# Optimization experiments

Hardware: AMD Instinct MI355X
Metric: run time of the kernel (lower is better)

The kernel has to match this reference:

```python
import jax, jax.numpy as jnp
import numpy as np

# column-index constants for the node feature matrix and edge attributes
VM, VA, PG, QG, PD, QD = 0, 1, 2, 3, 4, 5
G_COL, B_COL = 0, 1

N_NODES = 100000
N_EDGES = 3200000
N_FEAT = 6


def setup_inputs() -> dict:
    key = jax.random.key(0)
    k1, k2, k3, k4, k5, k6 = jax.random.split(key, 6)
    pred = jax.random.normal(k1, (N_NODES, N_FEAT), dtype=jnp.float32)
    target = jax.random.normal(k2, (N_NODES, N_FEAT), dtype=jnp.float32)
    src = jax.random.randint(k3, (N_EDGES,), 0, N_NODES, dtype=jnp.int32)
    dst = jax.random.randint(k4, (N_EDGES,), 0, N_NODES, dtype=jnp.int32)
    edge_index = jnp.stack([src, dst], axis=0)
    edge_attr = jax.random.normal(k5, (N_EDGES, 2), dtype=jnp.float32)
    mask = jax.random.bernoulli(k6, 0.5, (N_NODES, N_FEAT))
    return {"pred": pred, "target": target, "edge_index": edge_index,
            "edge_attr": edge_attr, "mask": mask}


def reference(pred, target, edge_index, edge_attr, mask):
    # temp_pred[~mask] = target[~mask]
    tp = jnp.where(mask, pred, target)

    V_m = tp[:, VM]
    V_a = tp[:, VA]
    V = V_m * jnp.exp(1j * V_a)           # complex64 [N]
    V_conj = jnp.conj(V)

    # conj(Y_bus) entries on edges: G - jB
    Y_conj = edge_attr[:, G_COL] - 1j * edge_attr[:, B_COL]  # complex64 [E]

    row, col = edge_index[0], edge_index[1]
    # (Y_bus_conj @ V_conj)[i] = sum over edges (i,j) of conj(Y_ij) * conj(V_j)
    msg = Y_conj * V_conj[col]                               # gather-multiply [E]
    matvec = jax.ops.segment_sum(msg, row, num_segments=tp.shape[0])  # scatter-add [N]

    S_injection = V * matvec                                  # diag(V) @ (...)

    net_P = tp[:, PG] - tp[:, PD]
    net_Q = tp[:, QG] - tp[:, QD]
    diff = (net_P + 1j * net_Q) - S_injection

    loss = jnp.mean(jnp.abs(diff))
    real_loss = jnp.mean(jnp.abs(jnp.real(diff)))
    imag_loss = jnp.mean(jnp.abs(jnp.imag(diff)))
    return (loss, real_loss, imag_loss)
```

## Files before the change

### kernel.cpp

```cpp
#include <hip/hip_runtime.h>
#include <hip/hip_fp16.h>
#include <math.h>

constexpr int N_NODES = 100000;
constexpr int N_EDGES = 3200000;
constexpr int NF      = 6;

constexpr int BSHIFT  = 10;
constexpr int BNODES  = 1 << BSHIFT;
constexpr int NB      = (N_NODES + BNODES - 1) >> BSHIFT;
constexpr int CAP     = 33792;
constexpr int NSLICE  = 8;
constexpr int TILE    = 2048;
constexpr int EPT     = TILE / 256;
constexpr int NBLK_PART = (N_EDGES + TILE - 1) / TILE;
constexpr int VPREP_BLOCKS = (N_NODES + 255) / 256;

constexpr size_t MV_BYTES = (size_t)NB * BNODES * 8;
constexpr size_t OFF_V    = 0;
constexpr size_t OFF_A    = OFF_V + (size_t)N_NODES * 8;
constexpr size_t OFF_L    = OFF_A + (size_t)NB * CAP * 8;
constexpr size_t OFF_MV   = OFF_L + (size_t)NB * CAP * 2;
constexpr size_t OFF_CNT  = OFF_MV + MV_BYTES;
constexpr size_t WS_NEED  = OFF_CNT + 1024;

union F2U { float2 f; unsigned long long u; };

__global__ __launch_bounds__(256) void node_prep(
        const float* __restrict__ pred,
        const float* __restrict__ target,
        const unsigned char* __restrict__ mask,
        float2* __restrict__ v,
        float* __restrict__ mv) {
    int i = blockIdx.x * blockDim.x + threadIdx.x;
    for (int k = i; k < NB * BNODES * 2; k += VPREP_BLOCKS * 256)
        mv[k] = 0.f;
    if (i >= N_NODES) return;
    const int b = i * NF;
    float vm = mask[b + 0] ? pred[b + 0] : target[b + 0];
    float va = mask[b + 1] ? pred[b + 1] : target[b + 1];
    float s, c;
    sincosf(va, &s, &c);
    v[i] = make_float2(vm * c, vm * s);
}

__global__ __launch_bounds__(256) void partition_edges(
        const int* __restrict__ row, const int* __restrict__ col,
        const float2* __restrict__ attr,
        const float2* __restrict__ v,
        unsigned int* __restrict__ gcur,
        float2* __restrict__ Ag,
        unsigned short* __restrict__ Lg) {
    __shared__ unsigned int h[4][NB];
    __shared__ unsigned int cur[4][NB];
    __shared__ int wb[4][NB];
    __shared__ int dbase[NB];
    __shared__ unsigned int tot_s[NB];
    __shared__ float2 rec_s[TILE];
    __shared__ unsigned short li_s[TILE];
    __shared__ unsigned char bkt_s[TILE];
    __shared__ int total_s;

    const int tid = threadIdx.x;
    const int w = tid >> 6;
    const int e0 = blockIdx.x * TILE;
    const int e_base = e0 + tid * EPT;
    const bool ok = e_base < N_EDGES;

    for (int i = tid; i < 4 * NB; i += 256) {
        (&h[0][0])[i] = 0u;
        (&cur[0][0])[i] = 0u;
    }
    __syncthreads();

    int r[EPT];
    if (ok) {
        int4 ra = *(const int4*)(row + e_base);
        int4 rb = *(const int4*)(row + e_base + 4);
        r[0]=ra.x; r[1]=ra.y; r[2]=ra.z; r[3]=ra.w;
        r[4]=rb.x; r[5]=rb.y; r[6]=rb.z; r[7]=rb.w;
        #pragma unroll
        for (int k = 0; k < EPT; ++k)
            atomicAdd(&h[w][r[k] >> BSHIFT], 1u);
    }
    __syncthreads();

    if (tid < NB)
        tot_s[tid] = h[0][tid] + h[1][tid] + h[2][tid] + h[3][tid];
    __syncthreads();

    if (tid < NB) {
        int lbase = 0;
        for (int j = 0; j < tid; ++j) lbase += (int)tot_s[j];
        unsigned t0 = h[0][tid], t1 = h[1][tid], t2 = h[2][tid];
        unsigned tot = tot_s[tid];
        unsigned g = tot ? atomicAdd(&gcur[tid], tot) : 0u;
        dbase[tid] = (int)g - lbase;
        wb[0][tid] = lbase;
        wb[1][tid] = lbase + (int)t0;
        wb[2][tid] = lbase + (int)(t0 + t1);
        wb[3][tid] = lbase + (int)(t0 + t1 + t2);
        if (tid == NB - 1) total_s = lbase + (int)tot;
    }
    __syncthreads();

    if (ok) {
        int4 ca = *(const int4*)(col + e_base);
        int4 cb = *(const int4*)(col + e_base + 4);
        int c[EPT] = {ca.x, ca.y, ca.z, ca.w, cb.x, cb.y, cb.z, cb.w};
        float2 vv[EPT];
        #pragma unroll
        for (int k = 0; k < EPT; ++k) vv[k] = v[c[k]];
        float4 a0 = *(const float4*)(attr + e_base);
        float4 a1 = *(const float4*)(attr + e_base + 2);
        float4 a2 = *(const float4*)(attr + e_base + 4);
        float4 a3 = *(const float4*)(attr + e_base + 6);
        float gx[EPT] = {a0.x, a0.z, a1.x, a1.z, a2.x, a2.z, a3.x, a3.z};
        float gy[EPT] = {a0.y, a0.w, a1.y, a1.w, a2.y, a2.w, a3.y, a3.w};
        #pragma unroll
        for (int k = 0; k < EPT; ++k) {
            int rr = r[k];
            int b = rr >> BSHIFT;
            int slot = wb[w][b] + (int)atomicAdd(&cur[w][b], 1u);
            float mre = fmaf(gx[k], vv[k].x, -gy[k] * vv[k].y);
            float mim = -fmaf(gx[k], vv[k].y, gy[k] * vv[k].x);
            rec_s[slot] = make_float2(mre, mim);
            li_s[slot]  = (unsigned short)(rr & (BNODES - 1));
            bkt_s[slot] = (unsigned char)b;
        }
    }
    __syncthreads();

    const int total = total_s;
    for (int j = tid; j < total; j += 256) {
        int b = (int)bkt_s[j];
        int g = dbase[b] + j;
        if (g < CAP) {
            size_t o = (size_t)b * CAP + g;
            Ag[o] = rec_s[j];
            Lg[o] = li_s[j];
        }
    }
}

__global__ __launch_bounds__(256) void accum_finalize(
        const unsigned int* __restrict__ gcur,
        const float2* __restrict__ Ag,
        const unsigned short* __restrict__ Lg,
        float* __restrict__ mv,
        unsigned int* __restrict__ sdone,
        float* __restrict__ sums,
        unsigned int* __restrict__ done_all,
        const float* __restrict__ pred,
        const float* __restrict__ target,
        const unsigned char* __restrict__ mask,
        const float2* __restrict__ v,
        float* __restrict__ out) {
    __shared__ float acc_re[BNODES];
    __shared__ float acc_im[BNODES];
    __shared__ unsigned int old_s;
    const int tid = threadIdx.x;
    const int b = blockIdx.x / NSLICE;
    const int s = blockIdx.x % NSLICE;
    int cnt = (int)min(gcur[b], (unsigned)CAP);
    for (int i = tid; i < BNODES; i += 256) { acc_re[i] = 0.f; acc_im[i] = 0.f; }
    __syncthreads();
    int per = (((cnt + NSLICE - 1) / NSLICE) + 3) & ~3;
    int st = s * per;
    int en = min(st + per, cnt);
    const float2* ap = Ag + (size_t)b * CAP;
    const unsigned short* lp = Lg + (size_t)b * CAP;
    int j = st + 4 * tid;
    for (; j + 3 < en; j += 1024) {
        float4 m01 = *(const float4*)(ap + j);
        float4 m23 = *(const float4*)(ap + j + 2);
        ushort4 l4 = *(const ushort4*)(lp + j);
        atomicAdd(&acc_re[l4.x], m01.x);
        atomicAdd(&acc_im[l4.x], m01.y);
        atomicAdd(&acc_re[l4.y], m01.z);
        atomicAdd(&acc_im[l4.y], m01.w);
        atomicAdd(&acc_re[l4.z], m23.x);
        atomicAdd(&acc_im[l4.z], m23.y);
        atomicAdd(&acc_re[l4.w], m23.z);
        atomicAdd(&acc_im[l4.w], m23.w);
    }
    for (; j < en; ++j) {
        float2 m = ap[j];
        int li = (int)lp[j];
        atomicAdd(&acc_re[li], m.x);
        atomicAdd(&acc_im[li], m.y);
    }
    __syncthreads();
    {
        float* mvb = mv + (((size_t)b << BSHIFT) << 1);
        for (int i = tid; i < BNODES; i += 256) {
            float r = acc_re[i];
            float q = acc_im[i];
            if (r != 0.f || q != 0.f) {
                atomicAdd(&mvb[2 * i],     r);
                atomicAdd(&mvb[2 * i + 1], q);
            }
        }
    }
    asm volatile("s_waitcnt vmcnt(0)" ::: "memory");
    __syncthreads();
    if (tid == 0)
        old_s = __hip_atomic_fetch_add(&sdone[b], 1u, __ATOMIC_RELAXED,
                                       __HIP_MEMORY_SCOPE_AGENT);
    __syncthreads();
    if (old_s != (unsigned)(NSLICE - 1)) return;

    const unsigned long long* pb =
        reinterpret_cast<const unsigned long long*>(mv) + ((size_t)b << BSHIFT);
    float a = 0.f, ar = 0.f, ai = 0.f;
    for (int li = tid; li < BNODES; li += 256) {
        int i = (b << BSHIFT) + li;
        if (i >= N_NODES) break;
        F2U cvt;
        cvt.u = __hip_atomic_load(&pb[li], __ATOMIC_RELAXED,
                                  __HIP_MEMORY_SCOPE_AGENT);
        float mr = cvt.f.x, mi = cvt.f.y;
        const int bb = i * NF;
        float pg = mask[bb + 2] ? pred[bb + 2] : target[bb + 2];
        float qg = mask[bb + 3] ? pred[bb + 3] : target[bb + 3];
        float pd = mask[bb + 4] ? pred[bb + 4] : target[bb + 4];
        float qd = mask[bb + 5] ? pred[bb + 5] : target[bb + 5];
        float netP = pg - pd;
        float netQ = qg - qd;
        float2 vv = v[i];
        float s_re = vv.x * mr - vv.y * mi;
        float s_im = vv.x * mi + vv.y * mr;
        float dre = netP - s_re;
        float dim = netQ - s_im;
        ar += fabsf(dre);
        ai += fabsf(dim);
        a  += sqrtf(dre * dre + dim * dim);
    }
    #pragma unroll
    for (int off = 32; off > 0; off >>= 1) {
        a  += __shfl_down(a,  off, 64);
        ar += __shfl_down(ar, off, 64);
        ai += __shfl_down(ai, off, 64);
    }
    __shared__ float red[3][4];
    int wave = tid >> 6;
    int lane = tid & 63;
    if (lane == 0) { red[0][wave] = a; red[1][wave] = ar; red[2][wave] = ai; }
    __syncthreads();
    if (tid == 0) {
        float r0 = atomicAdd(&sums[0], red[0][0] + red[0][1] + red[0][2] + red[0][3]);
        float r1 = atomicAdd(&sums[1], red[1][0] + red[1][1] + red[1][2] + red[1][3]);
        float r2 = atomicAdd(&sums[2], red[2][0] + red[2][1] + red[2][2] + red[2][3]);
        float chk = r0 + r1 + r2;
        if (chk == chk) {
            unsigned fin = atomicAdd(done_all, 1u);
            if (fin == (unsigned)(NB - 1)) {
                const float inv = 1.0f / (float)N_NODES;
                float t0 = atomicAdd(&sums[0], 0.f);
                float t1 = atomicAdd(&sums[1], 0.f);
                float t2 = atomicAdd(&sums[2], 0.f);
                __hip_atomic_store(&out[0], t0 * inv, __ATOMIC_RELAXED, __HIP_MEMORY_SCOPE_AGENT);
                __hip_atomic_store(&out[1], t1 * inv, __ATOMIC_RELAXED, __HIP_MEMORY_SCOPE_AGENT);
                __hip_atomic_store(&out[2], t2 * inv, __ATOMIC_RELAXED, __HIP_MEMORY_SCOPE_AGENT);
            }
        }
    }
}

__global__ void node_prep_fb(const float* __restrict__ pred,
                             const float* __restrict__ target,
                             const unsigned char* __restrict__ mask,
                             float2* __restrict__ v) {
    int i = blockIdx.x * blockDim.x + threadIdx.x;
    if (i >= N_NODES) return;
    const int b = i * NF;
    float vm = mask[b + 0] ? pred[b + 0] : target[b + 0];
    float va = mask[b + 1] ? pred[b + 1] : target[b + 1];
    float s, c;
    sincosf(va, &s, &c);
    v[i] = make_float2(vm * c, vm * s);
}

__global__ void edge_scatter_fb(const int* __restrict__ row,
                                const int* __restrict__ col,
                                const float2* __restrict__ attr,
                                const float2* __restrict__ v,
                                float2* __restrict__ mv) {
    int e = blockIdx.x * blockDim.x + threadIdx.x;
    if (e >= N_EDGES) return;
    int r = row[e];
    int c = col[e];
    float2 gb = attr[e];
    float2 vv = v[c];
    float mre = fmaf(gb.x, vv.x, -gb.y * vv.y);
    float mim = -fmaf(gb.x, vv.y, gb.y * vv.x);
    atomicAdd(&mv[r].x, mre);
    atomicAdd(&mv[r].y, mim);
}

__global__ void finalize_fb(const float* __restrict__ pred,
                            const float* __restrict__ target,
                            const unsigned char* __restrict__ mask,
                            const float2* __restrict__ v,
                            const float2* __restrict__ mv,
                            float* __restrict__ sums) {
    int i = blockIdx.x * blockDim.x + threadIdx.x;
    float a = 0.f, ar = 0.f, ai = 0.f;
    if (i < N_NODES) {
        const int b = i * NF;
        float pg = mask[b + 2] ? pred[b + 2] : target[b + 2];
        float qg = mask[b + 3] ? pred[b + 3] : target[b + 3];
        float pd = mask[b + 4] ? pred[b + 4] : target[b + 4];
        float qd = mask[b + 5] ? pred[b + 5] : target[b + 5];
        float netP = pg - pd;
        float netQ = qg - qd;
        float2 vv = v[i];
        float2 m = mv[i];
        float s_re = vv.x * m.x - vv.y * m.y;
        float s_im = vv.x * m.y + vv.y * m.x;
        float dre = netP - s_re;
        float dim = netQ - s_im;
        ar = fabsf(dre);
        ai = fabsf(dim);
        a  = sqrtf(dre * dre + dim * dim);
    }
    #pragma unroll
    for (int off = 32; off > 0; off >>= 1) {
        a  += __shfl_down(a,  off, 64);
        ar += __shfl_down(ar, off, 64);
        ai += __shfl_down(ai, off, 64);
    }
    __shared__ float red[3][4];
    int wave = threadIdx.x >> 6;
    int lane = threadIdx.x & 63;
    if (lane == 0) { red[0][wave] = a; red[1][wave] = ar; red[2][wave] = ai; }
    __syncthreads();
    if (threadIdx.x == 0) {
        atomicAdd(&sums[0], red[0][0] + red[0][1] + red[0][2] + red[0][3]);
        atomicAdd(&sums[1], red[1][0] + red[1][1] + red[1][2] + red[1][3]);
        atomicAdd(&sums[2], red[2][0] + red[2][1] + red[2][2] + red[2][3]);
    }
}

__global__ void write_out_fb(const float* __restrict__ sums, float* __restrict__ out) {
    if (threadIdx.x == 0 && blockIdx.x == 0) {
        const float inv = 1.0f / (float)N_NODES;
        out[0] = sums[0] * inv;
        out[1] = sums[1] * inv;
        out[2] = sums[2] * inv;
    }
}

extern "C" void kernel_launch(void* const* d_in, const int* in_sizes, int n_in,
                              void* d_out, int out_size, void* d_ws, size_t ws_size,
                              hipStream_t stream) {
    const float*         pred   = (const float*)d_in[0];
    const float*         target = (const float*)d_in[1];
    const int*           eidx   = (const int*)d_in[2];
    const float2*        attr   = (const float2*)d_in[3];
    const unsigned char* mask   = (const unsigned char*)d_in[4];
    float* out = (float*)d_out;

    const int* row = eidx;
    const int* col = eidx + N_EDGES;

    char* ws = (char*)d_ws;
    const int B = 256;

    if (ws_size >= WS_NEED) {
        float2*             v        = (float2*)(ws + OFF_V);
        float2*             Ag       = (float2*)(ws + OFF_A);
        unsigned short*     Lg       = (unsigned short*)(ws + OFF_L);
        float*              mv       = (float*)(ws + OFF_MV);
        unsigned int*       gcur     = (unsigned int*)(ws + OFF_CNT);
        unsigned int*       sdone    = (unsigned int*)(ws + OFF_CNT + 512);
        float*              sums     = (float*)(ws + OFF_CNT + 912);
        unsigned int*       done_all = (unsigned int*)(ws + OFF_CNT + 928);

        hipMemsetAsync(ws + OFF_CNT, 0, 1024, stream);
        node_prep<<<VPREP_BLOCKS, B, 0, stream>>>(pred, target, mask, v, mv);
        partition_edges<<<NBLK_PART, B, 0, stream>>>(row, col, attr, v,
                                                     gcur, Ag, Lg);
        accum_finalize<<<NB * NSLICE, B, 0, stream>>>(gcur, Ag, Lg, mv,
                                                      sdone, sums, done_all,
                                                      pred, target, mask, v, out);
    } else {
        float2* v    = (float2*)ws;
        float2* mv   = (float2*)(ws + (size_t)N_NODES * 8);
        float*  sums = (float*)(ws + 2ull * N_NODES * 8);
        hipMemsetAsync(mv, 0, (size_t)N_NODES * 8 + 16, stream);
        node_prep_fb<<<(N_NODES + B - 1) / B, B, 0, stream>>>(pred, target, mask, v);
        edge_scatter_fb<<<(N_EDGES + B - 1) / B, B, 0, stream>>>(row, col, attr, v, mv);
        finalize_fb<<<(N_NODES + B - 1) / B, B, 0, stream>>>(pred, target, mask, v, mv, sums);
        write_out_fb<<<1, 64, 0, stream>>>(sums, out);
    }
}
```

Before: 195.7 us.

## Replace bucketed edge partitioning with direct global float atomics scatter

Drops the two-pass scheme that bucketed edges by row block into a workspace and then reduced each bucket with LDS atomics. Each edge now computes its message and adds it straight into the global matvec using unsafeAtomicAdd (hardware float atomics). A separate per-node finalize kernel then does the reduction. The memset is removed and node loads are vectorised. This avoids writing and re-reading the staged buffer, but it sends about 6.4M random global atomics through L2.

```diff
diff --git a/kernel.cpp b/kernel.cpp
--- a/kernel.cpp
+++ b/kernel.cpp
@@ -1,240 +1,110 @@
 #include <hip/hip_runtime.h>
-#include <hip/hip_fp16.h>
 #include <math.h>
 
 constexpr int N_NODES = 100000;
 constexpr int N_EDGES = 3200000;
 constexpr int NF      = 6;
 
-constexpr int BSHIFT  = 10;
-constexpr int BNODES  = 1 << BSHIFT;
-constexpr int NB      = (N_NODES + BNODES - 1) >> BSHIFT;
-constexpr int CAP     = 33792;
-constexpr int NSLICE  = 8;
-constexpr int TILE    = 2048;
-constexpr int EPT     = TILE / 256;
-constexpr int NBLK_PART = (N_EDGES + TILE - 1) / TILE;
-constexpr int VPREP_BLOCKS = (N_NODES + 255) / 256;
-
-constexpr size_t MV_BYTES = (size_t)NB * BNODES * 8;
-constexpr size_t OFF_V    = 0;
-constexpr size_t OFF_A    = OFF_V + (size_t)N_NODES * 8;
-constexpr size_t OFF_L    = OFF_A + (size_t)NB * CAP * 8;
-constexpr size_t OFF_MV   = OFF_L + (size_t)NB * CAP * 2;
-constexpr size_t OFF_CNT  = OFF_MV + MV_BYTES;
-constexpr size_t WS_NEED  = OFF_CNT + 1024;
-
-union F2U { float2 f; unsigned long long u; };
+constexpr int EPT       = 4;
+constexpr int NP_BLOCKS = (N_NODES + 255) / 256;
+constexpr int ES_BLOCKS = (N_EDGES / EPT + 255) / 256;
+
+constexpr size_t OFF_V   = 0;
+constexpr size_t OFF_MV  = OFF_V  + (size_t)N_NODES * 8;
+constexpr size_t OFF_CNT = OFF_MV + (size_t)N_NODES * 8;
+constexpr size_t WS_NEED = OFF_CNT + 64;
+
+__device__ __forceinline__ void fadd_atomic(float* p, float v) {
+#if defined(__HIP_PLATFORM_AMD__)
+    unsafeAtomicAdd(p, v);
+#else
+    atomicAdd(p, v);
+#endif
+}
 
 __global__ __launch_bounds__(256) void node_prep(
         const float* __restrict__ pred,
         const float* __restrict__ target,
         const unsigned char* __restrict__ mask,
         float2* __restrict__ v,
-        float* __restrict__ mv) {
-    int i = blockIdx.x * blockDim.x + threadIdx.x;
-    for (int k = i; k < NB * BNODES * 2; k += VPREP_BLOCKS * 256)
-        mv[k] = 0.f;
+        float2* __restrict__ mv,
+        unsigned int* __restrict__ cnt) {
+    int i = blockIdx.x * 256 + threadIdx.x;
+    if (i < 8) cnt[i] = 0u;
     if (i >= N_NODES) return;
+    mv[i] = make_float2(0.f, 0.f);
     const int b = i * NF;
-    float vm = mask[b + 0] ? pred[b + 0] : target[b + 0];
-    float va = mask[b + 1] ? pred[b + 1] : target[b + 1];
+    uchar2 m01 = *(const uchar2*)(mask + b);
+    float2 p01 = *(const float2*)(pred + b);
+    float2 t01 = *(const float2*)(target + b);
+    float vm = m01.x ? p01.x : t01.x;
+    float va = m01.y ? p01.y : t01.y;
     float s, c;
     sincosf(va, &s, &c);
     v[i] = make_float2(vm * c, vm * s);
 }
 
-__global__ __launch_bounds__(256) void partition_edges(
-        const int* __restrict__ row, const int* __restrict__ col,
+__global__ __launch_bounds__(256) void edge_scatter(
+        const int* __restrict__ row,
+        const int* __restrict__ col,
         const float2* __restrict__ attr,
         const float2* __restrict__ v,
-        unsigned int* __restrict__ gcur,
-        float2* __restrict__ Ag,
-        unsigned short* __restrict__ Lg) {
-    __shared__ unsigned int h[4][NB];
-    __shared__ unsigned int cur[4][NB];
-    __shared__ int wb[4][NB];
-    __shared__ int dbase[NB];
-    __shared__ unsigned int tot_s[NB];
-    __shared__ float2 rec_s[TILE];
-    __shared__ unsigned short li_s[TILE];
-    __shared__ unsigned char bkt_s[TILE];
-    __shared__ int total_s;
-
-    const int tid = threadIdx.x;
-    const int w = tid >> 6;
-    const int e0 = blockIdx.x * TILE;
-    const int e_base = e0 + tid * EPT;
-    const bool ok = e_base < N_EDGES;
-
-    for (int i = tid; i < 4 * NB; i += 256) {
-        (&h[0][0])[i] = 0u;
-        (&cur[0][0])[i] = 0u;
-    }
-    __syncthreads();
-
-    int r[EPT];
-    if (ok) {
-        int4 ra = *(const int4*)(row + e_base);
-        int4 rb = *(const int4*)(row + e_base + 4);
-        r[0]=ra.x; r[1]=ra.y; r[2]=ra.z; r[3]=ra.w;
-        r[4]=rb.x; r[5]=rb.y; r[6]=rb.z; r[7]=rb.w;
-        #pragma unroll
-        for (int k = 0; k < EPT; ++k)
-            atomicAdd(&h[w][r[k] >> BSHIFT], 1u);
-    }
-    __syncthreads();
-
-    if (tid < NB)
-        tot_s[tid] = h[0][tid] + h[1][tid] + h[2][tid] + h[3][tid];
-    __syncthreads();
-
-    if (tid < NB) {
-        int lbase = 0;
-        for (int j = 0; j < tid; ++j) lbase += (int)tot_s[j];
-        unsigned t0 = h[0][tid], t1 = h[1][tid], t2 = h[2][tid];
-        unsigned tot = tot_s[tid];
-        unsigned g = tot ? atomicAdd(&gcur[tid], tot) : 0u;
-        dbase[tid] = (int)g - lbase;
-        wb[0][tid] = lbase;
-        wb[1][tid] = lbase + (int)t0;
-        wb[2][tid] = lbase + (int)(t0 + t1);
-        wb[3][tid] = lbase + (int)(t0 + t1 + t2);
-        if (tid == NB - 1) total_s = lbase + (int)tot;
-    }
-    __syncthreads();
-
-    if (ok) {
-        int4 ca = *(const int4*)(col + e_base);
-        int4 cb = *(const int4*)(col + e_base + 4);
-        int c[EPT] = {ca.x, ca.y, ca.z, ca.w, cb.x, cb.y, cb.z, cb.w};
-        float2 vv[EPT];
-        #pragma unroll
-        for (int k = 0; k < EPT; ++k) vv[k] = v[c[k]];
-        float4 a0 = *(const float4*)(attr + e_base);
-        float4 a1 = *(const float4*)(attr + e_base + 2);
-        float4 a2 = *(const float4*)(attr + e_base + 4);
-        float4 a3 = *(const float4*)(attr + e_base + 6);
-        float gx[EPT] = {a0.x, a0.z, a1.x, a1.z, a2.x, a2.z, a3.x, a3.z};
-        float gy[EPT] = {a0.y, a0.w, a1.y, a1.w, a2.y, a2.w, a3.y, a3.w};
-        #pragma unroll
-        for (int k = 0; k < EPT; ++k) {
-            int rr = r[k];
-            int b = rr >> BSHIFT;
-            int slot = wb[w][b] + (int)atomicAdd(&cur[w][b], 1u);
-            float mre = fmaf(gx[k], vv[k].x, -gy[k] * vv[k].y);
-            float mim = -fmaf(gx[k], vv[k].y, gy[k] * vv[k].x);
-            rec_s[slot] = make_float2(mre, mim);
-            li_s[slot]  = (unsigned short)(rr & (BNODES - 1));
-            bkt_s[slot] = (unsigned char)b;
-        }
-    }
-    __syncthreads();
-
-    const int total = total_s;
-    for (int j = tid; j < total; j += 256) {
-        int b = (int)bkt_s[j];
-        int g = dbase[b] + j;
-        if (g < CAP) {
-            size_t o = (size_t)b * CAP + g;
-            Ag[o] = rec_s[j];
-            Lg[o] = li_s[j];
-        }
-    }
-}
-
-__global__ __launch_bounds__(256) void accum_finalize(
-        const unsigned int* __restrict__ gcur,
-        const float2* __restrict__ Ag,
-        const unsigned short* __restrict__ Lg,
-        float* __restrict__ mv,
-        unsigned int* __restrict__ sdone,
-        float* __restrict__ sums,
-        unsigned int* __restrict__ done_all,
+        float2* __restrict__ mv) {
+    int t = blockIdx.x * 256 + threadIdx.x;
+    int e = t * EPT;
+    if (e >= N_EDGES) return;
+    int4   r4  = *(const int4*)(row + e);
+    int4   c4  = *(const int4*)(col + e);
+    float4 a01 = *(const float4*)(attr + e);
+    float4 a23 = *(const float4*)(attr + e + 2);
+    float2 v0 = v[c4.x];
+    float2 v1 = v[c4.y];
+    float2 v2 = v[c4.z];
+    float2 v3 = v[c4.w];
+    float* m = (float*)mv;
+    fadd_atomic(&m[2 * r4.x],      fmaf(a01.x, v0.x, -a01.y * v0.y));
+    fadd_atomic(&m[2 * r4.x + 1], -fmaf(a01.x, v0.y,  a01.y * v0.x));
+    fadd_atomic(&m[2 * r4.y],      fmaf(a01.z, v1.x, -a01.w * v1.y));
+    fadd_atomic(&m[2 * r4.y + 1], -fmaf(a01.z, v1.y,  a01.w * v1.x));
+    fadd_atomic(&m[2 * r4.z],      fmaf(a23.x, v2.x, -a23.y * v2.y));
+    fadd_atomic(&m[2 * r4.z + 1], -fmaf(a23.x, v2.y,  a23.y * v2.x));
+    fadd_atomic(&m[2 * r4.w],      fmaf(a23.z, v3.x, -a23.w * v3.y));
+    fadd_atomic(&m[2 * r4.w + 1], -fmaf(a23.z, v3.y,  a23.w * v3.x));
+}
+
+__global__ __launch_bounds__(256) void finalize(
         const float* __restrict__ pred,
         const float* __restrict__ target,
         const unsigned char* __restrict__ mask,
         const float2* __restrict__ v,
+        const float2* __restrict__ mv,
+        float* __restrict__ sums,
+        unsigned int* __restrict__ done_all,
         float* __restrict__ out) {
-    __shared__ float acc_re[BNODES];
-    __shared__ float acc_im[BNODES];
-    __shared__ unsigned int old_s;
     const int tid = threadIdx.x;
-    const int b = blockIdx.x / NSLICE;
-    const int s = blockIdx.x % NSLICE;
-    int cnt = (int)min(gcur[b], (unsigned)CAP);
-    for (int i = tid; i < BNODES; i += 256) { acc_re[i] = 0.f; acc_im[i] = 0.f; }
-    __syncthreads();
-    int per = (((cnt + NSLICE - 1) / NSLICE) + 3) & ~3;
-    int st = s * per;
-    int en = min(st + per, cnt);
-    const float2* ap = Ag + (size_t)b * CAP;
-    const unsigned short* lp = Lg + (size_t)b * CAP;
-    int j = st + 4 * tid;
-    for (; j + 3 < en; j += 1024) {
-        float4 m01 = *(const float4*)(ap + j);
-        float4 m23 = *(const float4*)(ap + j + 2);
-        ushort4 l4 = *(const ushort4*)(lp + j);
-        atomicAdd(&acc_re[l4.x], m01.x);
-        atomicAdd(&acc_im[l4.x], m01.y);
-        atomicAdd(&acc_re[l4.y], m01.z);
-        atomicAdd(&acc_im[l4.y], m01.w);
-        atomicAdd(&acc_re[l4.z], m23.x);
-        atomicAdd(&acc_im[l4.z], m23.y);
-        atomicAdd(&acc_re[l4.w], m23.z);
-        atomicAdd(&acc_im[l4.w], m23.w);
-    }
-    for (; j < en; ++j) {
-        float2 m = ap[j];
-        int li = (int)lp[j];
-        atomicAdd(&acc_re[li], m.x);
-        atomicAdd(&acc_im[li], m.y);
-    }
-    __syncthreads();
-    {
-        float* mvb = mv + (((size_t)b << BSHIFT) << 1);
-        for (int i = tid; i < BNODES; i += 256) {
-            float r = acc_re[i];
-            float q = acc_im[i];
-            if (r != 0.f || q != 0.f) {
-                atomicAdd(&mvb[2 * i],     r);
-                atomicAdd(&mvb[2 * i + 1], q);
-            }
-        }
-    }
-    asm volatile("s_waitcnt vmcnt(0)" ::: "memory");
-    __syncthreads();
-    if (tid == 0)
-        old_s = __hip_atomic_fetch_add(&sdone[b], 1u, __ATOMIC_RELAXED,
-                                       __HIP_MEMORY_SCOPE_AGENT);
-    __syncthreads();
-    if (old_s != (unsigned)(NSLICE - 1)) return;
-
-    const unsigned long long* pb =
-        reinterpret_cast<const unsigned long long*>(mv) + ((size_t)b << BSHIFT);
+    int i = blockIdx.x * 256 + tid;
     float a = 0.f, ar = 0.f, ai = 0.f;
-    for (int li = tid; li < BNODES; li += 256) {
-        int i = (b << BSHIFT) + li;
-        if (i >= N_NODES) break;
-        F2U cvt;
-        cvt.u = __hip_atomic_load(&pb[li], __ATOMIC_RELAXED,
-                                  __HIP_MEMORY_SCOPE_AGENT);
-        float mr = cvt.f.x, mi = cvt.f.y;
-        const int bb = i * NF;
-        float pg = mask[bb + 2] ? pred[bb + 2] : target[bb + 2];
-        float qg = mask[bb + 3] ? pred[bb + 3] : target[bb + 3];
-        float pd = mask[bb + 4] ? pred[bb + 4] : target[bb + 4];
-        float qd = mask[bb + 5] ? pred[bb + 5] : target[bb + 5];
-        float netP = pg - pd;
-        float netQ = qg - qd;
+    if (i < N_NODES) {
+        const int b = i * NF;
+        uchar2 m23 = *(const uchar2*)(mask + b + 2);
+        uchar2 m45 = *(const uchar2*)(mask + b + 4);
+        float2 p23 = *(const float2*)(pred + b + 2);
+        float2 p45 = *(const float2*)(pred + b + 4);
+        float2 t23 = *(const float2*)(target + b + 2);
+        float2 t45 = *(const float2*)(target + b + 4);
+        float pg = m23.x ? p23.x : t23.x;
+        float qg = m23.y ? p23.y : t23.y;
+        float pd = m45.x ? p45.x : t45.x;
+        float qd = m45.y ? p45.y : t45.y;
         float2 vv = v[i];
-        float s_re = vv.x * mr - vv.y * mi;
-        float s_im = vv.x * mi + vv.y * mr;
-        float dre = netP - s_re;
-        float dim = netQ - s_im;
-        ar += fabsf(dre);
-        ai += fabsf(dim);
-        a  += sqrtf(dre * dre + dim * dim);
+        float2 mm = mv[i];
+        float s_re = vv.x * mm.x - vv.y * mm.y;
+        float s_im = vv.x * mm.y + vv.y * mm.x;
+        float dre = (pg - pd) - s_re;
+        float dim = (qg - qd) - s_im;
+        ar = fabsf(dre);
+        ai = fabsf(dim);
+        a  = sqrtf(dre * dre + dim * dim);
     }
     #pragma unroll
     for (int off = 32; off > 0; off >>= 1) {
@@ -254,7 +124,7 @@
         float chk = r0 + r1 + r2;
         if (chk == chk) {
             unsigned fin = atomicAdd(done_all, 1u);
-            if (fin == (unsigned)(NB - 1)) {
+            if (fin == (unsigned)(NP_BLOCKS - 1)) {
                 const float inv = 1.0f / (float)N_NODES;
                 float t0 = atomicAdd(&sums[0], 0.f);
                 float t1 = atomicAdd(&sums[1], 0.f);
@@ -368,22 +238,16 @@
     const int B = 256;
 
     if (ws_size >= WS_NEED) {
-        float2*             v        = (float2*)(ws + OFF_V);
-        float2*             Ag       = (float2*)(ws + OFF_A);
-        unsigned short*     Lg       = (unsigned short*)(ws + OFF_L);
-        float*              mv       = (float*)(ws + OFF_MV);
-        unsigned int*       gcur     = (unsigned int*)(ws + OFF_CNT);
-        unsigned int*       sdone    = (unsigned int*)(ws + OFF_CNT + 512);
-        float*              sums     = (float*)(ws + OFF_CNT + 912);
-        unsigned int*       done_all = (unsigned int*)(ws + OFF_CNT + 928);
-
-        hipMemsetAsync(ws + OFF_CNT, 0, 1024, stream);
-        node_prep<<<VPREP_BLOCKS, B, 0, stream>>>(pred, target, mask, v, mv);
-        partition_edges<<<NBLK_PART, B, 0, stream>>>(row, col, attr, v,
-                                                     gcur, Ag, Lg);
-        accum_finalize<<<NB * NSLICE, B, 0, stream>>>(gcur, Ag, Lg, mv,
-                                                      sdone, sums, done_all,
-                                                      pred, target, mask, v, out);
+        float2*       v        = (float2*)(ws + OFF_V);
+        float2*       mv       = (float2*)(ws + OFF_MV);
+        unsigned int* cnt      = (unsigned int*)(ws + OFF_CNT);
+        float*        sums     = (float*)(ws + OFF_CNT);
+        unsigned int* done_all = (unsigned int*)(ws + OFF_CNT + 16);
+
+        node_prep<<<NP_BLOCKS, B, 0, stream>>>(pred, target, mask, v, mv, cnt);
+        edge_scatter<<<ES_BLOCKS, B, 0, stream>>>(row, col, attr, v, mv);
+        finalize<<<NP_BLOCKS, B, 0, stream>>>(pred, target, mask, v, mv,
+                                              sums, done_all, out);
     } else {
         float2* v    = (float2*)ws;
         float2* mv   = (float2*)(ws + (size_t)N_NODES * 8);
```

Result: slower. 431.1 us (+120.3%).
